# Optimization experiments

Measured on AMD Instinct MI355X. Metric: run time of the kernel, lower is better.

Reference implementation:

```python
import jax, jax.numpy as jnp
import numpy as np

B, T, F, H, C = 256, 128, 784, 1024, 10
BN_EPS = 1e-3  # keras BatchNormalization default epsilon


def setup_inputs() -> dict:
    key = jax.random.key(0)
    ks = jax.random.split(key, 20)
    f32 = jnp.float32
    inp = {}
    inp["x"] = jax.random.normal(ks[0], (B, T, F), f32)
    # feature-extraction Dense (784 -> H), tanh activation inside Dense
    inp["W_fe"] = jax.random.normal(ks[1], (F, H), f32) * 0.03
    inp["b_fe"] = jnp.zeros((H,), f32)
    # BN after featext Dense (inference mode: moving stats)
    inp["gamma1"] = 1.0 + 0.1 * jax.random.normal(ks[2], (H,), f32)
    inp["beta1"] = 0.1 * jax.random.normal(ks[3], (H,), f32)
    inp["mean1"] = 0.1 * jax.random.normal(ks[4], (H,), f32)
    inp["var1"] = jax.random.uniform(ks[5], (H,), f32, 0.5, 1.5)
    # Peephole LSTM cell params; keras gate order: i, f, c, o
    inp["kernel"] = jax.random.normal(ks[6], (F // F * H, 4 * H), f32) * 0.03  # (H, 4H)
    inp["rec_kernel"] = jax.random.normal(ks[7], (H, 4 * H), f32) * 0.03
    # unit_forget_bias=True -> forget-gate bias initialized to 1
    inp["bias"] = jnp.concatenate([jnp.zeros((H,), f32), jnp.ones((H,), f32), jnp.zeros((2 * H,), f32)])
    inp["peep_i"] = 0.1 * jax.random.normal(ks[8], (H,), f32)
    inp["peep_f"] = 0.1 * jax.random.normal(ks[9], (H,), f32)
    inp["peep_o"] = 0.1 * jax.random.normal(ks[10], (H,), f32)
    # BN before logit Dense
    inp["gamma2"] = 1.0 + 0.1 * jax.random.normal(ks[11], (H,), f32)
    inp["beta2"] = 0.1 * jax.random.normal(ks[12], (H,), f32)
    inp["mean2"] = 0.1 * jax.random.normal(ks[13], (H,), f32)
    inp["var2"] = jax.random.uniform(ks[14], (H,), f32, 0.5, 1.5)
    # logit Dense (H -> C), no bias
    inp["W_out"] = jax.random.normal(ks[15], (H, C), f32) * 0.03
    return inp


def _bn(x, gamma, beta, mean, var):
    return (x - mean) * jax.lax.rsqrt(var + BN_EPS) * gamma + beta


def reference(x, W_fe, b_fe, gamma1, beta1, mean1, var1, kernel, rec_kernel, bias,
              peep_i, peep_f, peep_o, gamma2, beta2, mean2, var2, W_out):
    # fc_bn_act_featext: Dense(tanh) -> BN -> tanh
    feat = jnp.tanh(x @ W_fe + b_fe)            # (B, T, H)
    feat = jnp.tanh(_bn(feat, gamma1, beta1, mean1, var1))

    xs = jnp.transpose(feat, (1, 0, 2))         # (T, B, H) for scan

    def step(carry, x_t):
        h, c = carry
        z = x_t @ kernel + h @ rec_kernel + bias  # (B, 4H)
        zi, zf, zc, zo = jnp.split(z, 4, axis=-1)
        i = jax.nn.sigmoid(zi + c * peep_i)
        f = jax.nn.sigmoid(zf + c * peep_f)
        c_new = f * c + i * jnp.tanh(zc)
        o = jax.nn.sigmoid(zo + c_new * peep_o)
        h_new = o * jnp.tanh(c_new)
        return (h_new, c_new), h_new

    init = (jnp.zeros((x.shape[0], H), x.dtype), jnp.zeros((x.shape[0], H), x.dtype))
    _, hs = jax.lax.scan(step, init, xs)         # (T, B, H)
    h_seq = jnp.transpose(hs, (1, 0, 2))         # (B, T, H)

    # bn_act_fc_logit: BN -> tanh -> Dense(no bias)
    y = jnp.tanh(_bn(h_seq, gamma2, beta2, mean2, var2))
    out = y @ W_out                              # (B, T, C)
    return out
```

## Files before the change

kernel.cpp:

```cpp
#include <hip/hip_runtime.h>

#define B_ 256
#define T_ 128
#define F_ 784
#define FP_ 800
#define H_ 1024
#define NG_ 4096
#define C_ 10
#define TC_ 16
#define MC_ (B_ * TC_)
#define BN_EPS 1e-3f

typedef short s16x8 __attribute__((ext_vector_type(8)));
typedef float f32x4 __attribute__((ext_vector_type(4)));
typedef unsigned long long u64;

__device__ __forceinline__ ushort f2bf(float f) {
    union { float f; unsigned u; } v; v.f = f;
    unsigned r = v.u + 0x7FFFu + ((v.u >> 16) & 1u);
    return (ushort)(r >> 16);
}
__device__ __forceinline__ float bf2f(ushort h) {
    union { unsigned u; float f; } v; v.u = ((unsigned)h) << 16;
    return v.f;
}
__device__ __forceinline__ float sigm(float x) {
    return 1.0f / (1.0f + __expf(-x));
}
__device__ __forceinline__ float fast_tanh(float x) {
    x = fminf(15.0f, fmaxf(-15.0f, x));
    float e = __expf(2.0f * x);
    return (e - 1.0f) / (e + 1.0f);
}
__device__ __forceinline__ void gl_lds16(const ushort* g, ushort* l) {
    __builtin_amdgcn_global_load_lds(
        (__attribute__((address_space(1))) void*)(g),
        (__attribute__((address_space(3))) void*)(l), 16, 0, 0);
}

__global__ __launch_bounds__(256) void prep_params(
    const float* __restrict__ gamma1, const float* __restrict__ beta1,
    const float* __restrict__ mean1, const float* __restrict__ var1,
    const float* __restrict__ gamma2, const float* __restrict__ beta2,
    const float* __restrict__ mean2, const float* __restrict__ var2,
    const float* __restrict__ W_out,
    float* __restrict__ sc1, float* __restrict__ sh1,
    float* __restrict__ sc2, float* __restrict__ sh2,
    ushort* __restrict__ woutT, float* __restrict__ c_buf, ushort* __restrict__ h_hist,
    unsigned* __restrict__ bar)
{
    int idx = blockIdx.x * 256 + threadIdx.x;
    if (idx < 1024) bar[idx] = 0u;
    if (idx < B_ * H_) { c_buf[idx] = 0.0f; h_hist[idx] = 0; }
    if (idx < H_) {
        float s1 = gamma1[idx] * rsqrtf(var1[idx] + BN_EPS);
        sc1[idx] = s1; sh1[idx] = beta1[idx] - mean1[idx] * s1;
        float s2 = gamma2[idx] * rsqrtf(var2[idx] + BN_EPS);
        sc2[idx] = s2; sh2[idx] = beta2[idx] - mean2[idx] * s2;
    }
    if (idx < 16 * H_) {
        int n = idx >> 10, k = idx & (H_ - 1);
        woutT[idx] = (n < C_) ? f2bf(W_out[k * C_ + n]) : (ushort)0;
    }
}

__global__ __launch_bounds__(256) void transpose_f32_to_bf16(
    const float* __restrict__ src, ushort* __restrict__ dst, int K, int N, int Kpad)
{
    __shared__ float tile[32][33];
    int tx = threadIdx.x & 31, ty = threadIdx.x >> 5;
    int bx = blockIdx.x, by = blockIdx.y;
    int col = bx * 32 + tx;
    for (int l = 0; l < 4; ++l) {
        int row = by * 32 + ty + l * 8;
        tile[ty + l * 8][tx] = (row < K && col < N) ? src[(long)row * N + col] : 0.0f;
    }
    __syncthreads();
    for (int l = 0; l < 4; ++l) {
        int n = bx * 32 + ty + l * 8;
        int k = by * 32 + tx;
        if (n < N && k < Kpad) dst[(long)n * Kpad + k] = f2bf(tile[tx][ty + l * 8]);
    }
}

__global__ __launch_bounds__(256) void transpose_perm_bf16(
    const float* __restrict__ src, ushort* __restrict__ dst)
{
    __shared__ float tile[32][33];
    int tx = threadIdx.x & 31, ty = threadIdx.x >> 5;
    int bx = blockIdx.x, by = blockIdx.y;
    int col = bx * 32 + tx;
    for (int l = 0; l < 4; ++l) {
        int row = by * 32 + ty + l * 8;
        tile[ty + l * 8][tx] = (row < H_) ? src[(long)row * NG_ + col] : 0.0f;
    }
    __syncthreads();
    for (int l = 0; l < 4; ++l) {
        int n = bx * 32 + ty + l * 8;
        int k = by * 32 + tx;
        int n2 = (n & (H_ - 1)) * 4 + (n >> 10);
        dst[(long)n2 * H_ + k] = f2bf(tile[tx][ty + l * 8]);
    }
}

__device__ __forceinline__ void convert_body(
    const float* __restrict__ x, ushort* __restrict__ xbf, int t0, int idx)
{
    int m = idx / 100;
    int kc = idx - m * 100;
    int b = m & (B_ - 1), tl = m >> 8;
    int k = kc * 8;
    ushort o[8];
    if (k < F_) {
        const float* src = x + ((long)b * T_ + t0 + tl) * F_ + k;
        float4 v0 = *(const float4*)src, v1 = *(const float4*)(src + 4);
        o[0]=f2bf(v0.x); o[1]=f2bf(v0.y); o[2]=f2bf(v0.z); o[3]=f2bf(v0.w);
        o[4]=f2bf(v1.x); o[5]=f2bf(v1.y); o[6]=f2bf(v1.z); o[7]=f2bf(v1.w);
    } else {
        for (int i = 0; i < 8; ++i) o[i] = 0;
    }
    *(uint4*)(xbf + (long)m * FP_ + k) = *(uint4*)o;
}

__global__ __launch_bounds__(256) void convert_x(
    const float* __restrict__ x, ushort* __restrict__ xbf, int t0)
{
    convert_body(x, xbf, t0, blockIdx.x * 256 + threadIdx.x);
}

__global__ __launch_bounds__(256, 2) void gemm1_c(
    const ushort* __restrict__ xbf, const ushort* __restrict__ wfeT,
    const float* __restrict__ b_fe, const float* __restrict__ sc1, const float* __restrict__ sh1,
    ushort* __restrict__ feat_c)
{
    __shared__ __align__(16) ushort As[64 * 32];
    __shared__ __align__(16) ushort Bs[128 * 32];
    int tid = threadIdx.x;
    int h = blockIdx.x;
    int L = (h & 7) * 64 + (h >> 3);
    int m0 = (L >> 3) * 64;
    int n0 = (L & 7) * 128;
    int wave = tid >> 6, lane = tid & 63;
    int wm = wave >> 1, wn = wave & 1;
    int l15 = lane & 15, quad = lane >> 4;

    f32x4 zero = {0.f, 0.f, 0.f, 0.f};
    f32x4 acc[2][4];
    for (int i = 0; i < 2; i++) for (int j = 0; j < 4; j++) acc[i][j] = zero;

    int srow = lane >> 2, kcol = (lane & 3) * 8;
    for (int kk = 0; kk < FP_ / 32; ++kk) {
        int kb = kk * 32;
        #pragma unroll
        for (int i = 0; i < 3; ++i) {
            int u = wave * 3 + i;
            int cr = ((u < 4) ? (u << 4) : ((u - 4) << 4)) + srow;
            const ushort* src = (u < 4) ? (xbf  + (long)(m0 + cr) * FP_ + kb + kcol)
                                        : (wfeT + (long)(n0 + cr) * FP_ + kb + kcol);
            ushort* dst = (u < 4) ? (As + (u * 64 + lane) * 8)
                                  : (Bs + ((u - 4) * 64 + lane) * 8);
            gl_lds16(src, dst);
        }
        __syncthreads();
        s16x8 af[2], bfr[4];
        for (int i = 0; i < 2; i++) af[i]  = *(const s16x8*)&As[(wm * 32 + i * 16 + l15) * 32 + quad * 8];
        for (int j = 0; j < 4; j++) bfr[j] = *(const s16x8*)&Bs[(wn * 64 + j * 16 + l15) * 32 + quad * 8];
        for (int i = 0; i < 2; i++)
            for (int j = 0; j < 4; j++)
                acc[i][j] = __builtin_amdgcn_mfma_f32_16x16x32_bf16(af[i], bfr[j], acc[i][j], 0, 0, 0);
        __syncthreads();
    }
    for (int j = 0; j < 4; j++) {
        int n_g = n0 + wn * 64 + j * 16 + l15;
        float bia = b_fe[n_g], s1 = sc1[n_g], sh = sh1[n_g];
        for (int i = 0; i < 2; i++) {
            int mb = m0 + wm * 32 + i * 16 + quad * 4;
            for (int r = 0; r < 4; r++) {
                float v = fast_tanh(acc[i][j][r] + bia);
                v = fast_tanh(v * s1 + sh);
                feat_c[(long)(mb + r) * H_ + n_g] = f2bf(v);
            }
        }
    }
}

__global__ __launch_bounds__(256) void gemm2_c(
    const ushort* __restrict__ feat_c, const ushort* __restrict__ kT2,
    ushort* __restrict__ zx_c)
{
    __shared__ __align__(16) ushort As[128 * 32];
    __shared__ __align__(16) ushort Bs[128 * 32];
    int tid = threadIdx.x;
    int h = blockIdx.x;
    int L = (h & 7) * 128 + (h >> 3);
    int st = L >> 6, s = L & 63;
    int m0 = ((st >> 2) * 8 + (s >> 3)) * 128;
    int n0 = ((st & 3) * 8 + (s & 7)) * 128;
    int wave = tid >> 6, lane = tid & 63;
    int wm = wave >> 1, wn = wave & 1;
    int l15 = lane & 15, quad = lane >> 4;

    f32x4 zero = {0.f, 0.f, 0.f, 0.f};
    f32x4 acc[4][4];
    for (int i = 0; i < 4; i++) for (int j = 0; j < 4; j++) acc[i][j] = zero;

    int srow = lane >> 2, kcol = (lane & 3) * 8;
    for (int kk = 0; kk < H_ / 32; ++kk) {
        int kb = kk * 32;
        #pragma unroll
        for (int i = 0; i < 4; ++i) {
            int c = wave * 4 + i;
            int cr = ((c & 7) << 4) + srow;
            const ushort* src = (c < 8) ? (feat_c + (long)(m0 + cr) * H_ + kb + kcol)
                                        : (kT2   + (long)(n0 + cr) * H_ + kb + kcol);
            ushort* dst = ((c < 8) ? As : Bs) + ((c & 7) << 9) + lane * 8;
            gl_lds16(src, dst);
        }
        __syncthreads();
        s16x8 af[4], bfr[4];
        for (int i = 0; i < 4; i++) af[i]  = *(const s16x8*)&As[(wm * 64 + i * 16 + l15) * 32 + quad * 8];
        for (int j = 0; j < 4; j++) bfr[j] = *(const s16x8*)&Bs[(wn * 64 + j * 16 + l15) * 32 + quad * 8];
        for (int i = 0; i < 4; i++)
            for (int j = 0; j < 4; j++)
                acc[i][j] = __builtin_amdgcn_mfma_f32_16x16x32_bf16(af[i], bfr[j], acc[i][j], 0, 0, 0);
        __syncthreads();
    }
    for (int j = 0; j < 4; j++) {
        int n_g = n0 + wn * 64 + j * 16 + l15;
        for (int i = 0; i < 4; i++) {
            int mb = m0 + wm * 64 + i * 16 + quad * 4;
            for (int r = 0; r < 4; r++)
                zx_c[(long)(mb + r) * NG_ + n_g] = f2bf(acc[i][j][r]);
        }
    }
}

__global__ __launch_bounds__(512, 2) void lstm_chunk(
    ushort* __restrict__ h_hist, float* __restrict__ c_buf,
    const ushort* __restrict__ rT2, const ushort* __restrict__ zx_c,
    const float* __restrict__ bias, const float* __restrict__ pi,
    const float* __restrict__ pf, const float* __restrict__ po,
    unsigned* __restrict__ bar, int ci)
{
    __shared__ __align__(16) ushort Hb[4][32 * 256];
    __shared__ float zbuf[128][33];
    int tid = threadIdx.x;
    int dom = blockIdx.x & 7;
    int nb  = blockIdx.x >> 3;
    int ub  = nb * 32;
    int m0  = dom * 32;
    unsigned* flags  = bar + dom * 8 * 16;
    unsigned* myFlag = bar + (dom * 8 + (nb >> 2)) * 16;

    int wave = tid >> 6, lane = tid & 63;
    int wn = wave;
    int l15 = lane & 15, quad = lane >> 4;

    int b2 = tid & 31, seg = tid >> 5;
    int gr = m0 + b2;
    float cst[2];
    *(float2*)cst = *(const float2*)(c_buf + (long)gr * H_ + ub + seg * 2);
    float bi2[2], bff[2], bc2[2], bo2[2], pI[2], pF[2], pO[2];
    for (int u = 0; u < 2; ++u) {
        int ug = ub + seg * 2 + u;
        bi2[u] = bias[ug];          bff[u] = bias[H_ + ug];
        bc2[u] = bias[2 * H_ + ug]; bo2[u] = bias[3 * H_ + ug];
        pI[u] = pi[ug]; pF[u] = pf[ug]; pO[u] = po[ug];
    }

    s16x8 rfrag[32];
    {
        const ushort* rbase = rT2 + (long)(ub * 4 + wn * 16 + l15) * H_ + quad * 8;
        #pragma unroll
        for (int kk = 0; kk < 32; ++kk)
            rfrag[kk] = *(const s16x8*)(rbase + kk * 32);
    }

    int srcoff[2], ldsoff[2];
    #pragma unroll
    for (int i = 0; i < 2; ++i) {
        int G  = i * 512 + tid;
        int sr = G >> 5;
        int sc = (G & 31) ^ (sr & 7);
        srcoff[i] = sr * H_ + sc * 8;
        ldsoff[i] = G * 8;
    }

    int r0 = l15;
    int rx = l15 & 7;
    asm volatile("s_waitcnt vmcnt(0)" ::: "memory");
    __syncthreads();

    for (int tl = 0; tl < TC_; ++tl) {
        int SG = ci * TC_ + tl;
        const ushort* hsrc = h_hist +
            (size_t)((tl == 0) ? (ci == 0 ? 0 : TC_) : tl) * (B_ * H_) + (size_t)m0 * H_;
        const ushort* zr = zx_c + ((size_t)tl * B_ + gr) * NG_ + (ub + seg * 2) * 4;
        union { uint4 u4; ushort s[8]; } zv;

        zv.u4 = *(const uint4*)zr;
        __builtin_amdgcn_sched_barrier(0);
        #pragma unroll
        for (int q = 0; q < 4; ++q) {
            #pragma unroll
            for (int i = 0; i < 2; ++i)
                gl_lds16(hsrc + srcoff[i] + q * 256, &Hb[q][0] + ldsoff[i]);
            __builtin_amdgcn_sched_barrier(0);
        }

        f32x4 acc0 = {0.f, 0.f, 0.f, 0.f}, acc1 = {0.f, 0.f, 0.f, 0.f};

#define SEG(E, VN) \
        asm volatile("s_waitcnt vmcnt(" #VN ") lgkmcnt(0)\n\ts_barrier" ::: "memory"); \
        __builtin_amdgcn_sched_barrier(0); \
        { \
            const ushort* bp = &Hb[E][0]; \
            _Pragma("unroll") \
            for (int kkl = 0; kkl < 8; ++kkl) { \
                s16x8 bfr = rfrag[(E) * 8 + kkl]; \
                int po_ = ((kkl * 4 + quad) ^ rx) << 3; \
                s16x8 a0v = *(const s16x8*)(bp + r0 * 256 + po_); \
                s16x8 a1v = *(const s16x8*)(bp + (r0 + 16) * 256 + po_); \
                acc0 = __builtin_amdgcn_mfma_f32_16x16x32_bf16(a0v, bfr, acc0, 0, 0, 0); \
                acc1 = __builtin_amdgcn_mfma_f32_16x16x32_bf16(a1v, bfr, acc1, 0, 0, 0); \
            } \
        }

        SEG(0, 6)
        SEG(1, 4)
        SEG(2, 2)
        SEG(3, 0)
#undef SEG

        #pragma unroll
        for (int r = 0; r < 4; ++r)
            zbuf[wn * 16 + l15][quad * 4 + r] = acc0[r];
        #pragma unroll
        for (int r = 0; r < 4; ++r)
            zbuf[wn * 16 + l15][16 + quad * 4 + r] = acc1[r];
        __syncthreads();

        ushort hnew[2];
        #pragma unroll
        for (int u = 0; u < 2; ++u) {
            int cb2 = (seg * 2 + u) * 4;
            float zi = zbuf[cb2 + 0][b2] + bi2[u] + bf2f(zv.s[u * 4 + 0]);
            float zf = zbuf[cb2 + 1][b2] + bff[u] + bf2f(zv.s[u * 4 + 1]);
            float zc = zbuf[cb2 + 2][b2] + bc2[u] + bf2f(zv.s[u * 4 + 2]);
            float zo = zbuf[cb2 + 3][b2] + bo2[u] + bf2f(zv.s[u * 4 + 3]);
            float co = cst[u];
            float ig = sigm(zi + co * pI[u]);
            float fg = sigm(zf + co * pF[u]);
            float cn = fg * co + ig * fast_tanh(zc);
            float og = sigm(zo + cn * pO[u]);
            cst[u] = cn;
            hnew[u] = f2bf(og * fast_tanh(cn));
        }
        union { ushort s[2]; unsigned w; } hv;
        hv.s[0] = hnew[0]; hv.s[1] = hnew[1];
        __hip_atomic_store(
            (unsigned*)(h_hist + (size_t)(tl + 1) * (B_ * H_) + (size_t)gr * H_ + ub + seg * 2),
            hv.w, __ATOMIC_RELAXED, __HIP_MEMORY_SCOPE_AGENT);

        __syncthreads();
        if (tid == 0)
            __hip_atomic_fetch_add(myFlag, 1u, __ATOMIC_RELAXED, __HIP_MEMORY_SCOPE_AGENT);
        if (tl < TC_ - 1) {
            if (tid < 8) {
                unsigned tgt = (unsigned)(SG + 1) * 4u;
                while (__hip_atomic_load(flags + tid * 16,
                           __ATOMIC_RELAXED, __HIP_MEMORY_SCOPE_AGENT) < tgt)
                    __builtin_amdgcn_s_sleep(1);
            }
            __syncthreads();
        }
    }
    *(float2*)(c_buf + (long)gr * H_ + ub + seg * 2) = *(float2*)cst;
}

__global__ __launch_bounds__(256) void final_convert(
    const ushort* __restrict__ h_hist, const ushort* __restrict__ woutT,
    const float* __restrict__ sc2, const float* __restrict__ sh2,
    float* __restrict__ out, int t0,
    const float* __restrict__ x, ushort* __restrict__ xbf, int t0n, int do_conv)
{
    int hb = blockIdx.x;
    int tid = threadIdx.x;
    if (hb >= 64) {
        if (do_conv)
            convert_body(x, xbf, t0n, (hb - 64) * 256 + tid);
        return;
    }
    __shared__ __align__(16) ushort As[64 * 40];
    __shared__ __align__(16) ushort Bs[16 * 40];
    long r0 = (long)hb * 64;
    const ushort* hbase = h_hist + (long)B_ * H_ + r0 * H_;
    int wave = tid >> 6, lane = tid & 63;
    int l15 = lane & 15, quad = lane >> 4;

    f32x4 acc = {0.f, 0.f, 0.f, 0.f};

    for (int kk = 0; kk < H_ / 32; ++kk) {
        int kb = kk * 32;
        {
            int row = tid >> 2, ch = tid & 3;
            int k = kb + ch * 8;
            union { uint4 u4; ushort s[8]; } in, ov;
            in.u4 = *(const uint4*)(hbase + (long)row * H_ + k);
            float4 sa = *(const float4*)(sc2 + k), sb = *(const float4*)(sc2 + k + 4);
            float4 ba = *(const float4*)(sh2 + k), bb = *(const float4*)(sh2 + k + 4);
            ov.s[0] = f2bf(fast_tanh(bf2f(in.s[0]) * sa.x + ba.x));
            ov.s[1] = f2bf(fast_tanh(bf2f(in.s[1]) * sa.y + ba.y));
            ov.s[2] = f2bf(fast_tanh(bf2f(in.s[2]) * sa.z + ba.z));
            ov.s[3] = f2bf(fast_tanh(bf2f(in.s[3]) * sa.w + ba.w));
            ov.s[4] = f2bf(fast_tanh(bf2f(in.s[4]) * sb.x + bb.x));
            ov.s[5] = f2bf(fast_tanh(bf2f(in.s[5]) * sb.y + bb.y));
            ov.s[6] = f2bf(fast_tanh(bf2f(in.s[6]) * sb.z + bb.z));
            ov.s[7] = f2bf(fast_tanh(bf2f(in.s[7]) * sb.w + bb.w));
            *(uint4*)&As[row * 40 + ch * 8] = ov.u4;
        }
        if (tid < 64) {
            int row = tid >> 2, ch = tid & 3;
            *(uint4*)&Bs[row * 40 + ch * 8] = *(const uint4*)(woutT + row * H_ + kb + ch * 8);
        }
        __syncthreads();
        s16x8 bfr = *(const s16x8*)&Bs[l15 * 40 + quad * 8];
        s16x8 af  = *(const s16x8*)&As[(wave * 16 + l15) * 40 + quad * 8];
        acc = __builtin_amdgcn_mfma_f32_16x16x32_bf16(af, bfr, acc, 0, 0, 0);
        __syncthreads();
    }
    if (l15 < C_) {
        for (int r = 0; r < 4; r++) {
            long rg = r0 + wave * 16 + quad * 4 + r;
            int tl = (int)(rg >> 8);
            int b  = (int)(rg & (B_ - 1));
            out[((long)b * T_ + t0 + tl) * C_ + l15] = acc[r];
        }
    }
}

extern "C" void kernel_launch(void* const* d_in, const int* in_sizes, int n_in,
                              void* d_out, int out_size, void* d_ws, size_t ws_size,
                              hipStream_t stream)
{
    const float* x       = (const float*)d_in[0];
    const float* W_fe    = (const float*)d_in[1];
    const float* b_fe    = (const float*)d_in[2];
    const float* gamma1  = (const float*)d_in[3];
    const float* beta1   = (const float*)d_in[4];
    const float* mean1   = (const float*)d_in[5];
    const float* var1    = (const float*)d_in[6];
    const float* kernelw = (const float*)d_in[7];
    const float* reck    = (const float*)d_in[8];
    const float* bias    = (const float*)d_in[9];
    const float* peep_i  = (const float*)d_in[10];
    const float* peep_f  = (const float*)d_in[11];
    const float* peep_o  = (const float*)d_in[12];
    const float* gamma2  = (const float*)d_in[13];
    const float* beta2   = (const float*)d_in[14];
    const float* mean2   = (const float*)d_in[15];
    const float* var2    = (const float*)d_in[16];
    const float* W_out   = (const float*)d_in[17];
    float* out = (float*)d_out;

    char* ws = (char*)d_ws;
    size_t o = 0;
    ushort* wfeT  = (ushort*)(ws + o); o += (size_t)H_ * FP_ * 2;
    ushort* kT2   = (ushort*)(ws + o); o += (size_t)NG_ * H_ * 2;
    ushort* rT2   = (ushort*)(ws + o); o += (size_t)NG_ * H_ * 2;
    ushort* xbf_c = (ushort*)(ws + o); o += (size_t)MC_ * FP_ * 2;
    ushort* feat_c= (ushort*)(ws + o); o += (size_t)MC_ * H_ * 2;
    ushort* zx_c  = (ushort*)(ws + o); o += (size_t)MC_ * NG_ * 2;
    ushort* h_hist= (ushort*)(ws + o); o += (size_t)(TC_ + 1) * B_ * H_ * 2;
    float*  c_buf = (float*)(ws + o);  o += (size_t)B_ * H_ * 4;
    float*  sc1   = (float*)(ws + o);  o += 4096;
    float*  sh1   = (float*)(ws + o);  o += 4096;
    float*  sc2   = (float*)(ws + o);  o += 4096;
    float*  sh2   = (float*)(ws + o);  o += 4096;
    ushort* woutT = (ushort*)(ws + o); o += 16 * H_ * 2;
    unsigned* bar = (unsigned*)(ws + o); o += 4096;

    prep_params<<<dim3(B_ * H_ / 256), dim3(256), 0, stream>>>(
        gamma1, beta1, mean1, var1, gamma2, beta2, mean2, var2, W_out,
        sc1, sh1, sc2, sh2, woutT, c_buf, h_hist, bar);

    transpose_f32_to_bf16<<<dim3(32, 25), dim3(256), 0, stream>>>(W_fe, wfeT, F_, H_, FP_);
    transpose_perm_bf16<<<dim3(128, 32), dim3(256), 0, stream>>>(kernelw, kT2);
    transpose_perm_bf16<<<dim3(128, 32), dim3(256), 0, stream>>>(reck, rT2);

    convert_x<<<dim3(MC_ * FP_ / 8 / 256), dim3(256), 0, stream>>>(x, xbf_c, 0);
    for (int ci = 0; ci < T_ / TC_; ++ci) {
        int t0 = ci * TC_;
        gemm1_c<<<dim3(512), dim3(256), 0, stream>>>(
            xbf_c, wfeT, b_fe, sc1, sh1, feat_c);
        gemm2_c<<<dim3(1024), dim3(256), 0, stream>>>(feat_c, kT2, zx_c);
        lstm_chunk<<<dim3(256), dim3(512), 0, stream>>>(
            h_hist, c_buf, rT2, zx_c, bias, peep_i, peep_f, peep_o, bar, ci);
        final_convert<<<dim3(64 + MC_ * FP_ / 8 / 256), dim3(256), 0, stream>>>(
            h_hist, woutT, sc2, sh2, out, t0,
            x, xbf_c, t0 + TC_, (ci < T_ / TC_ - 1) ? 1 : 0);
    }
}
```

Baseline: 1.940 ms.

## Overlap next-chunk feature GEMM with LSTM recurrence and pipeline h loads finer

Moves the next chunk's x conversion into the gemm2 launch and runs the next chunk's feature GEMM (gemm1) as extra blocks of the LSTM kernel, so they can use CUs left idle by the 256 persistent recurrent blocks. Only one gemm1 is launched before the loop. The LSTM's per-step h loading is split from 4 segments of 256 columns into 8 segments of 128, using a 4-slot ring buffer that is refilled while earlier slots are computed, which cuts LDS use to fit the shared smem. The risks are that the extra gemm1 blocks compete with the spin-waiting LSTM blocks for CUs and bandwidth, and that the finer segments need more barriers per step.

Measured after the change: 1.978 ms. No clear change (+2.0%).

```diff
diff --git a/kernel.cpp b/kernel.cpp
--- a/kernel.cpp
+++ b/kernel.cpp
@@ -128,19 +128,15 @@
     convert_body(x, xbf, t0, blockIdx.x * 256 + threadIdx.x);
 }
 
-__global__ __launch_bounds__(256, 2) void gemm1_c(
+__device__ __forceinline__ void gemm1_tile(
+    ushort* As, ushort* Bs, int ltid, int L,
     const ushort* __restrict__ xbf, const ushort* __restrict__ wfeT,
     const float* __restrict__ b_fe, const float* __restrict__ sc1, const float* __restrict__ sh1,
     ushort* __restrict__ feat_c)
 {
-    __shared__ __align__(16) ushort As[64 * 32];
-    __shared__ __align__(16) ushort Bs[128 * 32];
-    int tid = threadIdx.x;
-    int h = blockIdx.x;
-    int L = (h & 7) * 64 + (h >> 3);
     int m0 = (L >> 3) * 64;
     int n0 = (L & 7) * 128;
-    int wave = tid >> 6, lane = tid & 63;
+    int wave = ltid >> 6, lane = ltid & 63;
     int wm = wave >> 1, wn = wave & 1;
     int l15 = lane & 15, quad = lane >> 4;
 
@@ -184,15 +180,33 @@
     }
 }
 
-__global__ __launch_bounds__(256) void gemm2_c(
+__global__ __launch_bounds__(256, 2) void gemm1_c(
+    const ushort* __restrict__ xbf, const ushort* __restrict__ wfeT,
+    const float* __restrict__ b_fe, const float* __restrict__ sc1, const float* __restrict__ sh1,
+    ushort* __restrict__ feat_c)
+{
+    __shared__ __align__(16) ushort As[64 * 32];
+    __shared__ __align__(16) ushort Bs[128 * 32];
+    int h = blockIdx.x;
+    int L = (h & 7) * 64 + (h >> 3);
+    gemm1_tile(As, Bs, threadIdx.x, L, xbf, wfeT, b_fe, sc1, sh1, feat_c);
+}
+
+__global__ __launch_bounds__(256) void gemm2_conv(
     const ushort* __restrict__ feat_c, const ushort* __restrict__ kT2,
-    ushort* __restrict__ zx_c)
-{
+    ushort* __restrict__ zx_c,
+    const float* __restrict__ x, ushort* __restrict__ xbf, int t0n, int do_conv)
+{
+    int hb = blockIdx.x;
+    int tid = threadIdx.x;
+    if (hb >= 1024) {
+        if (do_conv)
+            convert_body(x, xbf, t0n, (hb - 1024) * 256 + tid);
+        return;
+    }
     __shared__ __align__(16) ushort As[128 * 32];
     __shared__ __align__(16) ushort Bs[128 * 32];
-    int tid = threadIdx.x;
-    int h = blockIdx.x;
-    int L = (h & 7) * 128 + (h >> 3);
+    int L = (hb & 7) * 128 + (hb >> 3);
     int st = L >> 6, s = L & 63;
     int m0 = ((st >> 2) * 8 + (s >> 3)) * 128;
     int n0 = ((st & 3) * 8 + (s & 7)) * 128;
@@ -235,16 +249,33 @@
     }
 }
 
-__global__ __launch_bounds__(512, 2) void lstm_chunk(
+__global__ __launch_bounds__(512, 2) void lstm_g1(
     ushort* __restrict__ h_hist, float* __restrict__ c_buf,
     const ushort* __restrict__ rT2, const ushort* __restrict__ zx_c,
     const float* __restrict__ bias, const float* __restrict__ pi,
     const float* __restrict__ pf, const float* __restrict__ po,
-    unsigned* __restrict__ bar, int ci)
-{
-    __shared__ __align__(16) ushort Hb[4][32 * 256];
-    __shared__ float zbuf[128][33];
+    unsigned* __restrict__ bar, int ci,
+    const ushort* __restrict__ xbf, const ushort* __restrict__ wfeT,
+    const float* __restrict__ b_fe, const float* __restrict__ sc1g,
+    const float* __restrict__ sh1g, ushort* __restrict__ feat_c, int do_g1)
+{
+    __shared__ __align__(16) char smem[49664];
     int tid = threadIdx.x;
+
+    if (blockIdx.x >= 256) {
+        if (do_g1) {
+            int b = blockIdx.x - 256;
+            int s = tid >> 8, ltid = tid & 255;
+            int L = (b & 7) * 64 + (b >> 3) * 2 + s;
+            ushort* As = (ushort*)(smem + s * 12288);
+            ushort* Bs = (ushort*)(smem + s * 12288 + 4096);
+            gemm1_tile(As, Bs, ltid, L, xbf, wfeT, b_fe, sc1g, sh1g, feat_c);
+        }
+        return;
+    }
+
+    ushort* HbBase = (ushort*)smem;
+    float*  zb     = (float*)(smem + 32768);
     int dom = blockIdx.x & 7;
     int nb  = blockIdx.x >> 3;
     int ub  = nb * 32;
@@ -276,14 +307,12 @@
             rfrag[kk] = *(const s16x8*)(rbase + kk * 32);
     }
 
-    int srcoff[2], ldsoff[2];
-    #pragma unroll
-    for (int i = 0; i < 2; ++i) {
-        int G  = i * 512 + tid;
-        int sr = G >> 5;
-        int sc = (G & 31) ^ (sr & 7);
-        srcoff[i] = sr * H_ + sc * 8;
-        ldsoff[i] = G * 8;
+    int srcoff, ldsoff;
+    {
+        int sr = tid >> 4;
+        int sc = (tid & 15) ^ (sr & 7);
+        srcoff = sr * H_ + sc * 8;
+        ldsoff = tid * 8;
     }
 
     int r0 = l15;
@@ -301,53 +330,58 @@
         zv.u4 = *(const uint4*)zr;
         __builtin_amdgcn_sched_barrier(0);
         #pragma unroll
-        for (int q = 0; q < 4; ++q) {
-            #pragma unroll
-            for (int i = 0; i < 2; ++i)
-                gl_lds16(hsrc + srcoff[i] + q * 256, &Hb[q][0] + ldsoff[i]);
+        for (int eq = 0; eq < 4; ++eq) {
+            gl_lds16(hsrc + srcoff + eq * 128, HbBase + eq * 4096 + ldsoff);
             __builtin_amdgcn_sched_barrier(0);
         }
 
         f32x4 acc0 = {0.f, 0.f, 0.f, 0.f}, acc1 = {0.f, 0.f, 0.f, 0.f};
 
-#define SEG(E, VN) \
+#define SEG(E, VN, REFILL) \
         asm volatile("s_waitcnt vmcnt(" #VN ") lgkmcnt(0)\n\ts_barrier" ::: "memory"); \
         __builtin_amdgcn_sched_barrier(0); \
+        if (REFILL) { \
+            gl_lds16(hsrc + srcoff + ((E) + 3) * 128, HbBase + (((E) - 1) & 3) * 4096 + ldsoff); \
+        } \
         { \
-            const ushort* bp = &Hb[E][0]; \
+            const ushort* bp = HbBase + ((E) & 3) * 4096; \
             _Pragma("unroll") \
-            for (int kkl = 0; kkl < 8; ++kkl) { \
-                s16x8 bfr = rfrag[(E) * 8 + kkl]; \
+            for (int kkl = 0; kkl < 4; ++kkl) { \
+                s16x8 bfr = rfrag[(E) * 4 + kkl]; \
                 int po_ = ((kkl * 4 + quad) ^ rx) << 3; \
-                s16x8 a0v = *(const s16x8*)(bp + r0 * 256 + po_); \
-                s16x8 a1v = *(const s16x8*)(bp + (r0 + 16) * 256 + po_); \
+                s16x8 a0v = *(const s16x8*)(bp + r0 * 128 + po_); \
+                s16x8 a1v = *(const s16x8*)(bp + (r0 + 16) * 128 + po_); \
                 acc0 = __builtin_amdgcn_mfma_f32_16x16x32_bf16(a0v, bfr, acc0, 0, 0, 0); \
                 acc1 = __builtin_amdgcn_mfma_f32_16x16x32_bf16(a1v, bfr, acc1, 0, 0, 0); \
             } \
         }
 
-        SEG(0, 6)
-        SEG(1, 4)
-        SEG(2, 2)
-        SEG(3, 0)
+        SEG(0, 3, 0)
+        SEG(1, 2, 1)
+        SEG(2, 2, 1)
+        SEG(3, 2, 1)
+        SEG(4, 2, 1)
+        SEG(5, 2, 0)
+        SEG(6, 1, 0)
+        SEG(7, 0, 0)
 #undef SEG
 
         #pragma unroll
         for (int r = 0; r < 4; ++r)
-            zbuf[wn * 16 + l15][quad * 4 + r] = acc0[r];
+            zb[(wn * 16 + l15) * 33 + quad * 4 + r] = acc0[r];
         #pragma unroll
         for (int r = 0; r < 4; ++r)
-            zbuf[wn * 16 + l15][16 + quad * 4 + r] = acc1[r];
+            zb[(wn * 16 + l15) * 33 + 16 + quad * 4 + r] = acc1[r];
         __syncthreads();
 
         ushort hnew[2];
         #pragma unroll
         for (int u = 0; u < 2; ++u) {
             int cb2 = (seg * 2 + u) * 4;
-            float zi = zbuf[cb2 + 0][b2] + bi2[u] + bf2f(zv.s[u * 4 + 0]);
-            float zf = zbuf[cb2 + 1][b2] + bff[u] + bf2f(zv.s[u * 4 + 1]);
-            float zc = zbuf[cb2 + 2][b2] + bc2[u] + bf2f(zv.s[u * 4 + 2]);
-            float zo = zbuf[cb2 + 3][b2] + bo2[u] + bf2f(zv.s[u * 4 + 3]);
+            float zi = zb[(cb2 + 0) * 33 + b2] + bi2[u] + bf2f(zv.s[u * 4 + 0]);
+            float zf = zb[(cb2 + 1) * 33 + b2] + bff[u] + bf2f(zv.s[u * 4 + 1]);
+            float zc = zb[(cb2 + 2) * 33 + b2] + bc2[u] + bf2f(zv.s[u * 4 + 2]);
+            float zo = zb[(cb2 + 3) * 33 + b2] + bo2[u] + bf2f(zv.s[u * 4 + 3]);
             float co = cst[u];
             float ig = sigm(zi + co * pI[u]);
             float fg = sigm(zf + co * pF[u]);
@@ -378,22 +412,15 @@
     *(float2*)(c_buf + (long)gr * H_ + ub + seg * 2) = *(float2*)cst;
 }
 
-__global__ __launch_bounds__(256) void final_convert(
+__global__ __launch_bounds__(256) void final_chunk(
     const ushort* __restrict__ h_hist, const ushort* __restrict__ woutT,
     const float* __restrict__ sc2, const float* __restrict__ sh2,
-    float* __restrict__ out, int t0,
-    const float* __restrict__ x, ushort* __restrict__ xbf, int t0n, int do_conv)
-{
-    int hb = blockIdx.x;
-    int tid = threadIdx.x;
-    if (hb >= 64) {
-        if (do_conv)
-            convert_body(x, xbf, t0n, (hb - 64) * 256 + tid);
-        return;
-    }
+    float* __restrict__ out, int t0)
+{
     __shared__ __align__(16) ushort As[64 * 40];
     __shared__ __align__(16) ushort Bs[16 * 40];
-    long r0 = (long)hb * 64;
+    int tid = threadIdx.x;
+    long r0 = (long)blockIdx.x * 64;
     const ushort* hbase = h_hist + (long)B_ * H_ + r0 * H_;
     int wave = tid >> 6, lane = tid & 63;
     int l15 = lane & 15, quad = lane >> 4;
@@ -489,15 +516,17 @@
     transpose_perm_bf16<<<dim3(128, 32), dim3(256), 0, stream>>>(reck, rT2);
 
     convert_x<<<dim3(MC_ * FP_ / 8 / 256), dim3(256), 0, stream>>>(x, xbf_c, 0);
+    gemm1_c<<<dim3(512), dim3(256), 0, stream>>>(xbf_c, wfeT, b_fe, sc1, sh1, feat_c);
+
     for (int ci = 0; ci < T_ / TC_; ++ci) {
         int t0 = ci * TC_;
-        gemm1_c<<<dim3(512), dim3(256), 0, stream>>>(
-            xbf_c, wfeT, b_fe, sc1, sh1, feat_c);
-        gemm2_c<<<dim3(1024), dim3(256), 0, stream>>>(feat_c, kT2, zx_c);
-        lstm_chunk<<<dim3(256), dim3(512), 0, stream>>>(
-            h_hist, c_buf, rT2, zx_c, bias, peep_i, peep_f, peep_o, bar, ci);
-        final_convert<<<dim3(64 + MC_ * FP_ / 8 / 256), dim3(256), 0, stream>>>(
-            h_hist, woutT, sc2, sh2, out, t0,
-            x, xbf_c, t0 + TC_, (ci < T_ / TC_ - 1) ? 1 : 0);
-    }
-}
+        int more = (ci < T_ / TC_ - 1) ? 1 : 0;
+        gemm2_conv<<<dim3(1024 + MC_ * FP_ / 8 / 256), dim3(256), 0, stream>>>(
+            feat_c, kT2, zx_c, x, xbf_c, t0 + TC_, more);
+        lstm_g1<<<dim3(512), dim3(512), 0, stream>>>(
+            h_hist, c_buf, rT2, zx_c, bias, peep_i, peep_f, peep_o, bar, ci,
+            xbf_c, wfeT, b_fe, sc1, sh1, feat_c, more);
+        final_chunk<<<dim3(MC_ / 64), dim3(256), 0, stream>>>(
+            h_hist, woutT, sc2, sh2, out, t0);
+    }
+}
```

## Software-pipeline chunks: fuse next-chunk x conversion into gemm2 and gemm1 into final kernel

Applied to the files above, without the earlier changes.

The per-chunk launch sequence is reorganised. The bf16 conversion of the next chunk's x now runs as extra blocks inside the gemm2 launch, and the next chunk's feature GEMM (gemm1) runs as extra blocks inside the final output-projection kernel. Only the first gemm1 is hoisted ahead of the loop. This cuts one kernel launch per chunk and fills idle CUs during the small final projection. It relies on zx_c being consumed before xbf is overwritten and on feat_c being free once gemm2 finishes, and it shares LDS between the two code paths.

Result: faster. 1.792 ms (-7.6%).

```diff
diff --git a/kernel.cpp b/kernel.cpp
--- a/kernel.cpp
+++ b/kernel.cpp
@@ -128,19 +128,15 @@
     convert_body(x, xbf, t0, blockIdx.x * 256 + threadIdx.x);
 }
 
-__global__ __launch_bounds__(256, 2) void gemm1_c(
+__device__ __forceinline__ void gemm1_tile(
+    ushort* As, ushort* Bs, int ltid, int L,
     const ushort* __restrict__ xbf, const ushort* __restrict__ wfeT,
     const float* __restrict__ b_fe, const float* __restrict__ sc1, const float* __restrict__ sh1,
     ushort* __restrict__ feat_c)
 {
-    __shared__ __align__(16) ushort As[64 * 32];
-    __shared__ __align__(16) ushort Bs[128 * 32];
-    int tid = threadIdx.x;
-    int h = blockIdx.x;
-    int L = (h & 7) * 64 + (h >> 3);
     int m0 = (L >> 3) * 64;
     int n0 = (L & 7) * 128;
-    int wave = tid >> 6, lane = tid & 63;
+    int wave = ltid >> 6, lane = ltid & 63;
     int wm = wave >> 1, wn = wave & 1;
     int l15 = lane & 15, quad = lane >> 4;
 
@@ -184,15 +180,33 @@
     }
 }
 
-__global__ __launch_bounds__(256) void gemm2_c(
+__global__ __launch_bounds__(256, 2) void gemm1_c(
+    const ushort* __restrict__ xbf, const ushort* __restrict__ wfeT,
+    const float* __restrict__ b_fe, const float* __restrict__ sc1, const float* __restrict__ sh1,
+    ushort* __restrict__ feat_c)
+{
+    __shared__ __align__(16) ushort As[64 * 32];
+    __shared__ __align__(16) ushort Bs[128 * 32];
+    int h = blockIdx.x;
+    int L = (h & 7) * 64 + (h >> 3);
+    gemm1_tile(As, Bs, threadIdx.x, L, xbf, wfeT, b_fe, sc1, sh1, feat_c);
+}
+
+__global__ __launch_bounds__(256) void gemm2_conv(
     const ushort* __restrict__ feat_c, const ushort* __restrict__ kT2,
-    ushort* __restrict__ zx_c)
-{
+    ushort* __restrict__ zx_c,
+    const float* __restrict__ x, ushort* __restrict__ xbf, int t0n, int do_conv)
+{
+    int hb = blockIdx.x;
+    int tid = threadIdx.x;
+    if (hb >= 1024) {
+        if (do_conv)
+            convert_body(x, xbf, t0n, (hb - 1024) * 256 + tid);
+        return;
+    }
     __shared__ __align__(16) ushort As[128 * 32];
     __shared__ __align__(16) ushort Bs[128 * 32];
-    int tid = threadIdx.x;
-    int h = blockIdx.x;
-    int L = (h & 7) * 128 + (h >> 3);
+    int L = (hb & 7) * 128 + (hb >> 3);
     int st = L >> 6, s = L & 63;
     int m0 = ((st >> 2) * 8 + (s >> 3)) * 128;
     int n0 = ((st & 3) * 8 + (s & 7)) * 128;
@@ -378,21 +392,27 @@
     *(float2*)(c_buf + (long)gr * H_ + ub + seg * 2) = *(float2*)cst;
 }
 
-__global__ __launch_bounds__(256) void final_convert(
+__global__ __launch_bounds__(256) void final_g1(
     const ushort* __restrict__ h_hist, const ushort* __restrict__ woutT,
     const float* __restrict__ sc2, const float* __restrict__ sh2,
     float* __restrict__ out, int t0,
-    const float* __restrict__ x, ushort* __restrict__ xbf, int t0n, int do_conv)
-{
+    const ushort* __restrict__ xbf, const ushort* __restrict__ wfeT,
+    const float* __restrict__ b_fe, const float* __restrict__ sc1,
+    const float* __restrict__ sh1, ushort* __restrict__ feat_c, int do_g1)
+{
+    __shared__ __align__(16) ushort smem[6144];
     int hb = blockIdx.x;
     int tid = threadIdx.x;
     if (hb >= 64) {
-        if (do_conv)
-            convert_body(x, xbf, t0n, (hb - 64) * 256 + tid);
+        if (do_g1) {
+            int b = hb - 64;
+            int L = (b & 7) * 64 + (b >> 3);
+            gemm1_tile(smem, smem + 2048, tid, L, xbf, wfeT, b_fe, sc1, sh1, feat_c);
+        }
         return;
     }
-    __shared__ __align__(16) ushort As[64 * 40];
-    __shared__ __align__(16) ushort Bs[16 * 40];
+    ushort* As = smem;
+    ushort* Bs = smem + 2560;
     long r0 = (long)hb * 64;
     const ushort* hbase = h_hist + (long)B_ * H_ + r0 * H_;
     int wave = tid >> 6, lane = tid & 63;
@@ -489,15 +509,17 @@
     transpose_perm_bf16<<<dim3(128, 32), dim3(256), 0, stream>>>(reck, rT2);
 
     convert_x<<<dim3(MC_ * FP_ / 8 / 256), dim3(256), 0, stream>>>(x, xbf_c, 0);
+    gemm1_c<<<dim3(512), dim3(256), 0, stream>>>(xbf_c, wfeT, b_fe, sc1, sh1, feat_c);
+
     for (int ci = 0; ci < T_ / TC_; ++ci) {
         int t0 = ci * TC_;
-        gemm1_c<<<dim3(512), dim3(256), 0, stream>>>(
-            xbf_c, wfeT, b_fe, sc1, sh1, feat_c);
-        gemm2_c<<<dim3(1024), dim3(256), 0, stream>>>(feat_c, kT2, zx_c);
+        int more = (ci < T_ / TC_ - 1) ? 1 : 0;
+        gemm2_conv<<<dim3(1024 + MC_ * FP_ / 8 / 256), dim3(256), 0, stream>>>(
+            feat_c, kT2, zx_c, x, xbf_c, t0 + TC_, more);
         lstm_chunk<<<dim3(256), dim3(512), 0, stream>>>(
             h_hist, c_buf, rT2, zx_c, bias, peep_i, peep_f, peep_o, bar, ci);
-        final_convert<<<dim3(64 + MC_ * FP_ / 8 / 256), dim3(256), 0, stream>>>(
+        final_g1<<<dim3(64 + 512), dim3(256), 0, stream>>>(
             h_hist, woutT, sc2, sh2, out, t0,
-            x, xbf_c, t0 + TC_, (ci < T_ / TC_ - 1) ? 1 : 0);
-    }
-}
+            xbf_c, wfeT, b_fe, sc1, sh1, feat_c, more);
+    }
+}
```
